# Performance work log

Measured on AMD Instinct MI355X. Metric: run time of the kernel, lower is better.

Reference implementation:

```python
import jax, jax.numpy as jnp
import numpy as np

N_NODES = 100000
N_EDGES = 1600000
IN_CH = 128
OUT_CH = 128


def setup_inputs() -> dict:
    key = jax.random.key(0)
    k1, k2, k3, k4, k5, k6 = jax.random.split(key, 6)
    x = jax.random.normal(k1, (N_NODES, IN_CH), dtype=jnp.float32)
    weight = jax.random.normal(k2, (IN_CH, OUT_CH), dtype=jnp.float32) * (1.0 / np.sqrt(IN_CH))
    bias = jax.random.uniform(k3, (OUT_CH,), dtype=jnp.float32)
    edge_row = jax.random.randint(k4, (N_EDGES,), 0, N_NODES, dtype=jnp.int64)
    edge_col = jax.random.randint(k5, (N_EDGES,), 0, N_NODES, dtype=jnp.int64)
    edge_weight = jax.random.uniform(k6, (N_EDGES,), dtype=jnp.float32)
    return {"x": x, "weight": weight, "bias": bias,
            "edge_row": edge_row, "edge_col": edge_col, "edge_weight": edge_weight}


def reference(x, weight, bias, edge_row, edge_col, edge_weight):
    # Dense transform: [N, in] @ [in, out] -> [N, out]
    h = x @ weight
    # SpMM: out[r] = sum_e w_e * h[c_e] for edges (r, c) -- gather + scatter-add
    msgs = edge_weight[:, None] * h[edge_col]          # [E, out]
    agg = jax.ops.segment_sum(msgs, edge_row, num_segments=N_NODES)  # [N, out]
    return agg + bias
```

## Files before the change

### kernel.cpp

```cpp
#include <hip/hip_runtime.h>

#define N_NODES 100000
#define N_EDGES_MAX 1600000
#define IN_CH 128
#define OUT_CH 128
#define NB 391
#define BLK_E 2048
#define NBLK_P 800
#define CAP_LDS 5120

typedef __attribute__((ext_vector_type(8))) short bf16x8_t;
typedef __attribute__((ext_vector_type(4))) float f32x4_t;

constexpr size_t align_up(size_t x) { return (x + 255) & ~size_t(255); }
constexpr size_t H_OFF     = 0;
constexpr size_t H_SZ      = (size_t)N_NODES * OUT_CH * 2;
constexpr size_t BREC_OFF  = align_up(H_OFF + H_SZ);
constexpr size_t BREC_SZ   = (size_t)N_EDGES_MAX * 8;
constexpr size_t SREC_OFF  = align_up(BREC_OFF + BREC_SZ);
constexpr size_t BLK_OFF   = align_up(SREC_OFF + BREC_SZ);
constexpr size_t BLK_SZ    = (size_t)NB * NBLK_P * 4;
constexpr size_t BTOT_OFF  = align_up(BLK_OFF + BLK_SZ);
constexpr size_t BTOT_SZ   = (size_t)NB * 4;
constexpr size_t BBASE_OFF = align_up(BTOT_OFF + BTOT_SZ);
constexpr size_t BBASE_SZ  = (size_t)(NB + 1) * 4;
constexpr size_t RS_OFF    = align_up(BBASE_OFF + BBASE_SZ);
constexpr size_t RS_SZ     = (size_t)(N_NODES + 1) * 4;
constexpr size_t WT_OFF    = align_up(RS_OFF + RS_SZ);
constexpr size_t WT_SZ     = (size_t)IN_CH * OUT_CH * 2;
constexpr size_t WS_NEED   = WT_OFF + WT_SZ;

__device__ __forceinline__ unsigned short f2bf(float f) {
    unsigned u = __float_as_uint(f);
    return (unsigned short)((u + 0x7FFFu + ((u >> 16) & 1u)) >> 16);
}
__device__ __forceinline__ float bf2f(unsigned short b) {
    return __uint_as_float((unsigned)b << 16);
}
__device__ __forceinline__ float bflo(unsigned u) { return __uint_as_float(u << 16); }
__device__ __forceinline__ float bfhi(unsigned u) { return __uint_as_float(u & 0xFFFF0000u); }

__device__ __forceinline__ void accum8(float4& a0, float4& a1, const uint4 hv,
                                       const float wt) {
    a0.x += wt * bflo(hv.x); a0.y += wt * bfhi(hv.x);
    a0.z += wt * bflo(hv.y); a0.w += wt * bfhi(hv.y);
    a1.x += wt * bflo(hv.z); a1.y += wt * bfhi(hv.z);
    a1.z += wt * bflo(hv.w); a1.w += wt * bfhi(hv.w);
}

__global__ __launch_bounds__(256) void prep_wt(const float* __restrict__ W,
                                               unsigned short* __restrict__ wt) {
    const int idx = blockIdx.x * 256 + threadIdx.x;
    const float w = W[idx];
    const int k = idx >> 7, c = idx & 127;
    wt[c * 128 + k] = f2bf(w);
}

__global__ __launch_bounds__(256) void gemm_mfma(const float* __restrict__ x,
                                                 const unsigned short* __restrict__ wt,
                                                 unsigned short* __restrict__ h) {
    const int wv = threadIdx.x >> 6;
    const int l  = threadIdx.x & 63;
    const int lr = l & 15;
    const int lk = (l >> 4) * 8;
    const long rbase = (long)blockIdx.x * 64 + wv * 16;

    f32x4_t acc[8];
#pragma unroll
    for (int i = 0; i < 8; ++i) acc[i] = (f32x4_t){0.f, 0.f, 0.f, 0.f};

    long arow = rbase + lr;
    if (arow >= N_NODES) arow = N_NODES - 1;
    const float4* xr = (const float4*)(x + arow * IN_CH);

    for (int kc = 0; kc < 128; kc += 32) {
        float4 f0 = xr[(kc + lk) >> 2];
        float4 f1 = xr[((kc + lk) >> 2) + 1];
        bf16x8_t a;
        a[0] = (short)f2bf(f0.x); a[1] = (short)f2bf(f0.y);
        a[2] = (short)f2bf(f0.z); a[3] = (short)f2bf(f0.w);
        a[4] = (short)f2bf(f1.x); a[5] = (short)f2bf(f1.y);
        a[6] = (short)f2bf(f1.z); a[7] = (short)f2bf(f1.w);
#pragma unroll
        for (int ct = 0; ct < 8; ++ct) {
            bf16x8_t b = *(const bf16x8_t*)&wt[(size_t)(ct * 16 + lr) * 128 + kc + lk];
            acc[ct] = __builtin_amdgcn_mfma_f32_16x16x32_bf16(a, b, acc[ct], 0, 0, 0);
        }
    }

    const int r0 = (l >> 4) * 4;
#pragma unroll
    for (int ct = 0; ct < 8; ++ct) {
        const int col = ct * 16 + lr;
#pragma unroll
        for (int reg = 0; reg < 4; ++reg) {
            long r = rbase + r0 + reg;
            if (r < N_NODES) h[r * OUT_CH + col] = f2bf(acc[ct][reg]);
        }
    }
}

__global__ __launch_bounds__(256) void bucket_hist(const int* __restrict__ erow,
                                                   unsigned* __restrict__ blkcnt,
                                                   int n) {
    __shared__ unsigned cnt[NB];
    const int t = threadIdx.x, p = blockIdx.x;
    for (int i = t; i < NB; i += 256) cnt[i] = 0u;
    __syncthreads();
    const int e0 = p * BLK_E;
#pragma unroll
    for (int j = 0; j < 8; ++j) {
        int e = e0 + j * 256 + t;
        if (e < n) atomicAdd(&cnt[(unsigned)erow[e] >> 8], 1u);
    }
    __syncthreads();
    for (int i = t; i < NB; i += 256) blkcnt[(size_t)i * NBLK_P + p] = cnt[i];
}

__global__ __launch_bounds__(256) void scan_col(unsigned* __restrict__ blkcnt,
                                                unsigned* __restrict__ btotal,
                                                int nblk) {
    __shared__ unsigned part[256];
    const int b = blockIdx.x, t = threadIdx.x;
    unsigned* col = blkcnt + (size_t)b * NBLK_P;
    unsigned v[4];
    unsigned sum = 0;
    const int p0 = t * 4;
#pragma unroll
    for (int j = 0; j < 4; ++j) {
        int p = p0 + j;
        v[j] = (p < nblk) ? col[p] : 0u;
        sum += v[j];
    }
    part[t] = sum;
    __syncthreads();
    for (int off = 1; off < 256; off <<= 1) {
        unsigned a = (t >= off) ? part[t - off] : 0u;
        __syncthreads();
        part[t] += a;
        __syncthreads();
    }
    unsigned excl = part[t] - sum;
#pragma unroll
    for (int j = 0; j < 4; ++j) {
        int p = p0 + j;
        if (p < nblk) { unsigned tv = v[j]; col[p] = excl; excl += tv; }
    }
    if (t == 255) btotal[b] = part[255];
}

__global__ __launch_bounds__(512) void scan_buckets(const unsigned* __restrict__ btotal,
                                                    unsigned* __restrict__ bbase,
                                                    unsigned* __restrict__ row_start,
                                                    int n_edges) {
    __shared__ unsigned s[512];
    const int t = threadIdx.x;
    unsigned v = (t < NB) ? btotal[t] : 0u;
    s[t] = v;
    __syncthreads();
    for (int off = 1; off < 512; off <<= 1) {
        unsigned a = (t >= off) ? s[t - off] : 0u;
        __syncthreads();
        s[t] += a;
        __syncthreads();
    }
    if (t < NB) bbase[t] = s[t] - v;
    if (t == 0) {
        bbase[NB] = (unsigned)n_edges;
        row_start[N_NODES] = (unsigned)n_edges;
    }
}

__global__ __launch_bounds__(256) void bucket_scatter(const int* __restrict__ erow,
                                                      const int* __restrict__ ecol,
                                                      const float* __restrict__ ew,
                                                      const unsigned* __restrict__ blkbase,
                                                      const unsigned* __restrict__ bbase,
                                                      uint2* __restrict__ brec,
                                                      int n) {
    __shared__ unsigned cnt[NB];
    __shared__ unsigned basec[NB];
    const int t = threadIdx.x, p = blockIdx.x;
    for (int i = t; i < NB; i += 256) {
        cnt[i] = 0u;
        basec[i] = bbase[i] + blkbase[(size_t)i * NBLK_P + p];
    }
    __syncthreads();
    const int e0 = p * BLK_E;
#pragma unroll
    for (int j = 0; j < 8; ++j) {
        int e = e0 + j * 256 + t;
        if (e < n) {
            unsigned r = (unsigned)erow[e];
            unsigned c = (unsigned)ecol[e];
            float w = ew[e];
            unsigned bk = r >> 8;
            unsigned rank = atomicAdd(&cnt[bk], 1u);
            brec[basec[bk] + rank] =
                make_uint2(((r & 255u) << 17) | c, __float_as_uint(w));
        }
    }
}

__global__ __launch_bounds__(256) void row_scatter(const uint2* __restrict__ brec,
                                                   const unsigned* __restrict__ bbase,
                                                   unsigned* __restrict__ row_start,
                                                   uint2* __restrict__ srec) {
    __shared__ unsigned hist[256], sc[256], cur[256];
    __shared__ uint2 recs[CAP_LDS];
    const int b = blockIdx.x, t = threadIdx.x;
    const unsigned s = bbase[b], e = bbase[b + 1];
    const unsigned m = e - s;
    hist[t] = 0u;
    __syncthreads();
    const bool fits = (m <= CAP_LDS);
    if (fits) {
        for (unsigned i = t; i < m; i += 256) {
            uint2 rc = brec[s + i];
            recs[i] = rc;
            atomicAdd(&hist[rc.x >> 17], 1u);
        }
    } else {
        for (unsigned i = t; i < m; i += 256)
            atomicAdd(&hist[brec[s + i].x >> 17], 1u);
    }
    __syncthreads();
    unsigned v = hist[t];
    sc[t] = v;
    __syncthreads();
    for (int off = 1; off < 256; off <<= 1) {
        unsigned a = (t >= off) ? sc[t - off] : 0u;
        __syncthreads();
        sc[t] += a;
        __syncthreads();
    }
    const unsigned gpos = s + sc[t] - v;
    const int grow = b * 256 + t;
    if (grow < N_NODES) row_start[grow] = gpos;
    cur[t] = gpos;
    __syncthreads();
    if (fits) {
        for (unsigned i = t; i < m; i += 256) {
            uint2 rc = recs[i];
            unsigned pos = atomicAdd(&cur[rc.x >> 17], 1u);
            srec[pos] = make_uint2(rc.x & 0x1FFFFu, rc.y);
        }
    } else {
        for (unsigned i = t; i < m; i += 256) {
            uint2 rc = brec[s + i];
            unsigned pos = atomicAdd(&cur[rc.x >> 17], 1u);
            srec[pos] = make_uint2(rc.x & 0x1FFFFu, rc.y);
        }
    }
}

__global__ __launch_bounds__(256) void aggregate(const unsigned short* __restrict__ h,
                                                 const uint2* __restrict__ srec,
                                                 const unsigned* __restrict__ row_start,
                                                 const float* __restrict__ bias,
                                                 float* __restrict__ out) {
    const int t = threadIdx.x, lane = t & 15;
    const int r = blockIdx.x * 16 + (t >> 4);
    if (r >= N_NODES) return;
    const unsigned s = row_start[r], e = row_start[r + 1];

    const float4* b4 = (const float4*)bias;
    float4 a0 = b4[lane * 2];
    float4 a1 = b4[lane * 2 + 1];

    const uint4* h16 = (const uint4*)h;

    unsigned i = s;
    for (; i + 4 <= e; i += 4) {
        uint2 r0 = srec[i];
        uint2 r1 = srec[i + 1];
        uint2 r2 = srec[i + 2];
        uint2 r3 = srec[i + 3];
        uint4 v0 = h16[(size_t)r0.x * 16 + lane];
        uint4 v1 = h16[(size_t)r1.x * 16 + lane];
        uint4 v2 = h16[(size_t)r2.x * 16 + lane];
        uint4 v3 = h16[(size_t)r3.x * 16 + lane];
        accum8(a0, a1, v0, __uint_as_float(r0.y));
        accum8(a0, a1, v1, __uint_as_float(r1.y));
        accum8(a0, a1, v2, __uint_as_float(r2.y));
        accum8(a0, a1, v3, __uint_as_float(r3.y));
    }
    for (; i < e; ++i) {
        uint2 rc = srec[i];
        uint4 vv = h16[(size_t)rc.x * 16 + lane];
        accum8(a0, a1, vv, __uint_as_float(rc.y));
    }

    float4* o = (float4*)(out + (size_t)r * OUT_CH + lane * 8);
    o[0] = a0;
    o[1] = a1;
}

__global__ __launch_bounds__(256) void gemm_xw(const float* __restrict__ x,
                                               const float* __restrict__ W,
                                               unsigned short* __restrict__ h) {
    __shared__ float Wl[128 * 128];
    __shared__ float Xl[32 * 128];
    const int t = threadIdx.x;
    const float4* W4 = (const float4*)W;
    float4* Wl4 = (float4*)Wl;
#pragma unroll
    for (int i = 0; i < 16; ++i) Wl4[t + 256 * i] = W4[t + 256 * i];
    const long rbase = (long)blockIdx.x * 32;
    const float4* x4 = (const float4*)(x + rbase * IN_CH);
    float4* Xl4 = (float4*)Xl;
#pragma unroll
    for (int i = 0; i < 4; ++i) Xl4[t + 256 * i] = x4[t + 256 * i];
    __syncthreads();
    const int tx = t & 31;
    const int ty = t >> 5;
    float acc[4][4];
#pragma unroll
    for (int i = 0; i < 4; ++i)
#pragma unroll
        for (int j = 0; j < 4; ++j) acc[i][j] = 0.f;
    for (int k = 0; k < 128; ++k) {
        float4 w = *(const float4*)&Wl[k * 128 + tx * 4];
        float xv[4];
#pragma unroll
        for (int i = 0; i < 4; ++i) xv[i] = Xl[(ty * 4 + i) * 128 + k];
#pragma unroll
        for (int i = 0; i < 4; ++i) {
            acc[i][0] += xv[i] * w.x;
            acc[i][1] += xv[i] * w.y;
            acc[i][2] += xv[i] * w.z;
            acc[i][3] += xv[i] * w.w;
        }
    }
#pragma unroll
    for (int i = 0; i < 4; ++i) {
        long r = rbase + ty * 4 + i;
        ushort4 o;
        o.x = f2bf(acc[i][0]); o.y = f2bf(acc[i][1]);
        o.z = f2bf(acc[i][2]); o.w = f2bf(acc[i][3]);
        *(ushort4*)&h[r * OUT_CH + tx * 4] = o;
    }
}

__global__ __launch_bounds__(256) void init_bias(float* __restrict__ out,
                                                 const float* __restrict__ bias) {
    int idx = blockIdx.x * 256 + threadIdx.x;
    float4 b = ((const float4*)bias)[idx & 31];
    ((float4*)out)[idx] = b;
}

__global__ __launch_bounds__(256) void spmm_scatter(const unsigned short* __restrict__ h,
                                                    const int* __restrict__ erow,
                                                    const int* __restrict__ ecol,
                                                    const float* __restrict__ ew,
                                                    float* __restrict__ out,
                                                    int n_edges) {
    const int t = threadIdx.x;
    const int lane = t & 31;
    const int e = blockIdx.x * 8 + (t >> 5);
    if (e >= n_edges) return;
    const int r = erow[e];
    const int c = ecol[e];
    const float w = ew[e];
    ushort4 hv = ((const ushort4*)(h + (size_t)c * OUT_CH))[lane];
    float* o = out + (size_t)r * OUT_CH + lane * 4;
    atomicAdd(o + 0, w * bf2f(hv.x));
    atomicAdd(o + 1, w * bf2f(hv.y));
    atomicAdd(o + 2, w * bf2f(hv.z));
    atomicAdd(o + 3, w * bf2f(hv.w));
}

extern "C" void kernel_launch(void* const* d_in, const int* in_sizes, int n_in,
                              void* d_out, int out_size, void* d_ws, size_t ws_size,
                              hipStream_t stream) {
    const float* x    = (const float*)d_in[0];
    const float* W    = (const float*)d_in[1];
    const float* bias = (const float*)d_in[2];
    const int*   erow = (const int*)d_in[3];
    const int*   ecol = (const int*)d_in[4];
    const float* ew   = (const float*)d_in[5];
    float* out = (float*)d_out;
    const int n_edges = in_sizes[3];

    char* ws = (char*)d_ws;
    unsigned short* h  = (unsigned short*)(ws + H_OFF);
    uint2*    brec     = (uint2*)(ws + BREC_OFF);
    uint2*    srec     = (uint2*)(ws + SREC_OFF);
    unsigned* blkcnt   = (unsigned*)(ws + BLK_OFF);
    unsigned* btotal   = (unsigned*)(ws + BTOT_OFF);
    unsigned* bbase    = (unsigned*)(ws + BBASE_OFF);
    unsigned* rowstart = (unsigned*)(ws + RS_OFF);
    unsigned short* wt = (unsigned short*)(ws + WT_OFF);

    const int nblk = (n_edges + BLK_E - 1) / BLK_E;
    if (ws_size >= WS_NEED && n_edges <= N_EDGES_MAX) {
        prep_wt<<<64, 256, 0, stream>>>(W, wt);
        gemm_mfma<<<(N_NODES + 63) / 64, 256, 0, stream>>>(x, wt, h);
        bucket_hist<<<nblk, 256, 0, stream>>>(erow, blkcnt, n_edges);
        scan_col<<<NB, 256, 0, stream>>>(blkcnt, btotal, nblk);
        scan_buckets<<<1, 512, 0, stream>>>(btotal, bbase, rowstart, n_edges);
        bucket_scatter<<<nblk, 256, 0, stream>>>(erow, ecol, ew, blkcnt, bbase,
                                                 brec, n_edges);
        row_scatter<<<NB, 256, 0, stream>>>(brec, bbase, rowstart, srec);
        aggregate<<<(N_NODES + 15) / 16, 256, 0, stream>>>(h, srec, rowstart,
                                                           bias, out);
    } else {
        gemm_xw<<<N_NODES / 32, 256, 0, stream>>>(x, W, h);
        init_bias<<<(N_NODES * 32) / 256, 256, 0, stream>>>(out, bias);
        spmm_scatter<<<(n_edges + 7) / 8, 256, 0, stream>>>(h, erow, ecol, ew,
                                                            out, n_edges);
    }
}
```

Measured before the change: 155.6 us.

## Fold weight prep into GEMM LDS and use wave-per-row aggregation with dynamic rows

The separate prep_wt kernel is removed. Each GEMM block now loads W, converts it to bf16 and stores it transposed into padded shared memory, which saves a launch but repeats the W conversion in every block. The aggregate kernel now gives each 64-lane wave a whole row, with each lane holding 2 channels, and waves pull the next row from a shared atomic counter to balance uneven row degrees. This trades 16-byte gathers per lane for 4-byte gathers per lane across a full wave.

New measurement: 170.0 us. 1.09x slower.

```diff
diff --git a/kernel.cpp b/kernel.cpp
--- a/kernel.cpp
+++ b/kernel.cpp
@@ -8,6 +8,7 @@
 #define BLK_E 2048
 #define NBLK_P 800
 #define CAP_LDS 5120
+#define ROWS_PB 32
 
 typedef __attribute__((ext_vector_type(8))) short bf16x8_t;
 typedef __attribute__((ext_vector_type(4))) float f32x4_t;
@@ -26,9 +27,7 @@
 constexpr size_t BBASE_SZ  = (size_t)(NB + 1) * 4;
 constexpr size_t RS_OFF    = align_up(BBASE_OFF + BBASE_SZ);
 constexpr size_t RS_SZ     = (size_t)(N_NODES + 1) * 4;
-constexpr size_t WT_OFF    = align_up(RS_OFF + RS_SZ);
-constexpr size_t WT_SZ     = (size_t)IN_CH * OUT_CH * 2;
-constexpr size_t WS_NEED   = WT_OFF + WT_SZ;
+constexpr size_t WS_NEED   = RS_OFF + RS_SZ;
 
 __device__ __forceinline__ unsigned short f2bf(float f) {
     unsigned u = __float_as_uint(f);
@@ -40,27 +39,29 @@
 __device__ __forceinline__ float bflo(unsigned u) { return __uint_as_float(u << 16); }
 __device__ __forceinline__ float bfhi(unsigned u) { return __uint_as_float(u & 0xFFFF0000u); }
 
-__device__ __forceinline__ void accum8(float4& a0, float4& a1, const uint4 hv,
-                                       const float wt) {
-    a0.x += wt * bflo(hv.x); a0.y += wt * bfhi(hv.x);
-    a0.z += wt * bflo(hv.y); a0.w += wt * bfhi(hv.y);
-    a1.x += wt * bflo(hv.z); a1.y += wt * bfhi(hv.z);
-    a1.z += wt * bflo(hv.w); a1.w += wt * bfhi(hv.w);
-}
-
-__global__ __launch_bounds__(256) void prep_wt(const float* __restrict__ W,
-                                               unsigned short* __restrict__ wt) {
-    const int idx = blockIdx.x * 256 + threadIdx.x;
-    const float w = W[idx];
-    const int k = idx >> 7, c = idx & 127;
-    wt[c * 128 + k] = f2bf(w);
-}
-
 __global__ __launch_bounds__(256) void gemm_mfma(const float* __restrict__ x,
-                                                 const unsigned short* __restrict__ wt,
+                                                 const float* __restrict__ W,
                                                  unsigned short* __restrict__ h) {
-    const int wv = threadIdx.x >> 6;
-    const int l  = threadIdx.x & 63;
+    __shared__ unsigned short WTl[128 * 136];
+    const int t = threadIdx.x;
+
+    const float4* W4 = (const float4*)W;
+#pragma unroll
+    for (int i = 0; i < 16; ++i) {
+        const int idx = t + 256 * i;
+        float4 v = W4[idx];
+        const int base = idx * 4;
+        const int k = base >> 7;
+        const int c = base & 127;
+        WTl[(c + 0) * 136 + k] = f2bf(v.x);
+        WTl[(c + 1) * 136 + k] = f2bf(v.y);
+        WTl[(c + 2) * 136 + k] = f2bf(v.z);
+        WTl[(c + 3) * 136 + k] = f2bf(v.w);
+    }
+    __syncthreads();
+
+    const int wv = t >> 6;
+    const int l  = t & 63;
     const int lr = l & 15;
     const int lk = (l >> 4) * 8;
     const long rbase = (long)blockIdx.x * 64 + wv * 16;
@@ -83,7 +84,7 @@
         a[6] = (short)f2bf(f1.z); a[7] = (short)f2bf(f1.w);
 #pragma unroll
         for (int ct = 0; ct < 8; ++ct) {
-            bf16x8_t b = *(const bf16x8_t*)&wt[(size_t)(ct * 16 + lr) * 128 + kc + lk];
+            bf16x8_t b = *(const bf16x8_t*)&WTl[(ct * 16 + lr) * 136 + kc + lk];
             acc[ct] = __builtin_amdgcn_mfma_f32_16x16x32_bf16(a, b, acc[ct], 0, 0, 0);
         }
     }
@@ -259,41 +260,54 @@
                                                  const unsigned* __restrict__ row_start,
                                                  const float* __restrict__ bias,
                                                  float* __restrict__ out) {
-    const int t = threadIdx.x, lane = t & 15;
-    const int r = blockIdx.x * 16 + (t >> 4);
-    if (r >= N_NODES) return;
-    const unsigned s = row_start[r], e = row_start[r + 1];
-
-    const float4* b4 = (const float4*)bias;
-    float4 a0 = b4[lane * 2];
-    float4 a1 = b4[lane * 2 + 1];
-
-    const uint4* h16 = (const uint4*)h;
-
-    unsigned i = s;
-    for (; i + 4 <= e; i += 4) {
-        uint2 r0 = srec[i];
-        uint2 r1 = srec[i + 1];
-        uint2 r2 = srec[i + 2];
-        uint2 r3 = srec[i + 3];
-        uint4 v0 = h16[(size_t)r0.x * 16 + lane];
-        uint4 v1 = h16[(size_t)r1.x * 16 + lane];
-        uint4 v2 = h16[(size_t)r2.x * 16 + lane];
-        uint4 v3 = h16[(size_t)r3.x * 16 + lane];
-        accum8(a0, a1, v0, __uint_as_float(r0.y));
-        accum8(a0, a1, v1, __uint_as_float(r1.y));
-        accum8(a0, a1, v2, __uint_as_float(r2.y));
-        accum8(a0, a1, v3, __uint_as_float(r3.y));
-    }
-    for (; i < e; ++i) {
-        uint2 rc = srec[i];
-        uint4 vv = h16[(size_t)rc.x * 16 + lane];
-        accum8(a0, a1, vv, __uint_as_float(rc.y));
-    }
-
-    float4* o = (float4*)(out + (size_t)r * OUT_CH + lane * 8);
-    o[0] = a0;
-    o[1] = a1;
+    __shared__ unsigned cntw;
+    const int t = threadIdx.x;
+    const int ln = t & 63;
+    const int wv = t >> 6;
+    if (t == 0) cntw = 4u;
+    __syncthreads();
+
+    const float2 bv = ((const float2*)bias)[ln];
+    const unsigned* h32 = (const unsigned*)h;
+
+    int rl = wv;
+    while (rl < ROWS_PB) {
+        const long r = (long)blockIdx.x * ROWS_PB + rl;
+        if (r < N_NODES) {
+            unsigned i = row_start[r];
+            const unsigned e = row_start[r + 1];
+            float ax = bv.x, ay = bv.y;
+            for (; i + 4 <= e; i += 4) {
+                uint2 r0 = srec[i];
+                uint2 r1 = srec[i + 1];
+                uint2 r2 = srec[i + 2];
+                uint2 r3 = srec[i + 3];
+                unsigned v0 = h32[(size_t)r0.x * 64 + ln];
+                unsigned v1 = h32[(size_t)r1.x * 64 + ln];
+                unsigned v2 = h32[(size_t)r2.x * 64 + ln];
+                unsigned v3 = h32[(size_t)r3.x * 64 + ln];
+                float w0 = __uint_as_float(r0.y);
+                float w1 = __uint_as_float(r1.y);
+                float w2 = __uint_as_float(r2.y);
+                float w3 = __uint_as_float(r3.y);
+                ax += w0 * bflo(v0); ay += w0 * bfhi(v0);
+                ax += w1 * bflo(v1); ay += w1 * bfhi(v1);
+                ax += w2 * bflo(v2); ay += w2 * bfhi(v2);
+                ax += w3 * bflo(v3); ay += w3 * bfhi(v3);
+            }
+            for (; i < e; ++i) {
+                uint2 rc = srec[i];
+                unsigned v = h32[(size_t)rc.x * 64 + ln];
+                float w = __uint_as_float(rc.y);
+                ax += w * bflo(v); ay += w * bfhi(v);
+            }
+            ((float2*)out)[r * 64 + ln] = make_float2(ax, ay);
+        }
+        unsigned nxt = 0u;
+        if (ln == 0) nxt = atomicAdd(&cntw, 1u);
+        nxt = __shfl(nxt, 0);
+        rl = (int)nxt;
+    }
 }
 
 __global__ __launch_bounds__(256) void gemm_xw(const float* __restrict__ x,
@@ -390,20 +404,18 @@
     unsigned* btotal   = (unsigned*)(ws + BTOT_OFF);
     unsigned* bbase    = (unsigned*)(ws + BBASE_OFF);
     unsigned* rowstart = (unsigned*)(ws + RS_OFF);
-    unsigned short* wt = (unsigned short*)(ws + WT_OFF);
 
     const int nblk = (n_edges + BLK_E - 1) / BLK_E;
     if (ws_size >= WS_NEED && n_edges <= N_EDGES_MAX) {
-        prep_wt<<<64, 256, 0, stream>>>(W, wt);
-        gemm_mfma<<<(N_NODES + 63) / 64, 256, 0, stream>>>(x, wt, h);
+        gemm_mfma<<<(N_NODES + 63) / 64, 256, 0, stream>>>(x, W, h);
         bucket_hist<<<nblk, 256, 0, stream>>>(erow, blkcnt, n_edges);
         scan_col<<<NB, 256, 0, stream>>>(blkcnt, btotal, nblk);
         scan_buckets<<<1, 512, 0, stream>>>(btotal, bbase, rowstart, n_edges);
         bucket_scatter<<<nblk, 256, 0, stream>>>(erow, ecol, ew, blkcnt, bbase,
                                                  brec, n_edges);
         row_scatter<<<NB, 256, 0, stream>>>(brec, bbase, rowstart, srec);
-        aggregate<<<(N_NODES + 15) / 16, 256, 0, stream>>>(h, srec, rowstart,
-                                                           bias, out);
+        aggregate<<<(N_NODES + ROWS_PB - 1) / ROWS_PB, 256, 0, stream>>>(
+            h, srec, rowstart, bias, out);
     } else {
         gemm_xw<<<N_NODES / 32, 256, 0, stream>>>(x, W, h);
         init_bias<<<(N_NODES * 32) / 256, 256, 0, stream>>>(out, bias);
```
